# Performance work log

Hardware: AMD Instinct MI355X
Metric: run time of the kernel (lower is better)

The kernel has to match this reference:

```python
import jax, jax.numpy as jnp
import numpy as np

VEC_DIM = 128
N_DOCS = 100000
N_WORDS = 100000
BATCH = 16384
CTX = 8
N_SAMPLES = 6


def setup_inputs() -> dict:
    key = jax.random.key(0)
    k1, k2, k3, k4, k5 = jax.random.split(key, 5)
    doc_ids = jax.random.randint(k1, (BATCH,), 0, N_DOCS, dtype=jnp.int64 if jax.config.jax_enable_x64 else jnp.int32)
    context_ids = jax.random.randint(k2, (BATCH, CTX), 0, N_WORDS)
    sample_ids = jax.random.randint(k3, (BATCH, N_SAMPLES), 0, N_WORDS)
    paragraph_matrix = jax.random.normal(k4, (N_DOCS, VEC_DIM), dtype=jnp.float32)
    word_matrix = jax.random.normal(k5, (N_WORDS, VEC_DIM), dtype=jnp.float32)
    outputs = jnp.zeros((VEC_DIM, N_WORDS), dtype=jnp.float32)
    return {
        "doc_ids": doc_ids,
        "context_ids": context_ids,
        "sample_ids": sample_ids,
        "paragraph_matrix": paragraph_matrix,
        "word_matrix": word_matrix,
        "outputs": outputs,
    }


def reference(doc_ids, context_ids, sample_ids, paragraph_matrix, word_matrix, outputs):
    # concat=False branch of DistributedMemory.forward
    # [B, CTX, D] gathered then summed over context -> [B, D]
    word_sum = jnp.sum(word_matrix[context_ids, :], axis=1)
    doc_vec = paragraph_matrix[doc_ids, :]            # [B, D]
    inputs = doc_vec + word_sum                       # [B, D]
    # outputs[:, sample_ids] -> [D, B, S]; bmm([B,1,D],[B,D,S]) == einsum
    out_cols = outputs[:, sample_ids]                 # [D, B, S]
    logits = jnp.einsum("bd,dbs->bs", inputs, out_cols)  # [B, S]
    return logits
```

## Files before the change

kernel.cpp:

```cpp
#include <hip/hip_runtime.h>
#include <stdint.h>

#define VEC_DIM   128
#define N_WORDS   100000
#define CTX       8
#define N_SAMPLES 6
#define BATCH     16384
#define N_GROUPS  6250
#define TOTAL_S   (BATCH * N_SAMPLES)
#define CAP       64

static constexpr size_t OFF_INPUTS  = 0;
static constexpr size_t OFF_COUNT   = 8388608;
static constexpr size_t OFF_RECORDS = OFF_COUNT + 25024;

__global__ void k_zero(uint32_t* __restrict__ count) {
    int i = blockIdx.x * 256 + threadIdx.x;
    if (i < N_GROUPS) count[i] = 0u;
}

__global__ __launch_bounds__(256) void k_gather_append(
    const int* __restrict__ doc_ids, const int* __restrict__ context_ids,
    const int* __restrict__ sample_ids,
    const float* __restrict__ para, const float* __restrict__ words,
    float* __restrict__ inputs, uint32_t* __restrict__ count,
    uint32_t* __restrict__ records)
{
    const int t    = threadIdx.x;
    const int wave = t >> 6;
    const int lane = t & 63;
    const int b    = blockIdx.x * 4 + wave;

    if (t < 24) {
        int i  = blockIdx.x * 24 + t;
        int id = sample_ids[i];
        int g  = id >> 4;
        uint32_t pos = atomicAdd(&count[g], 1u);
        int bb = i / N_SAMPLES;
        int ss = i - bb * N_SAMPLES;
        if (pos < CAP)
            records[g * CAP + pos] =
                ((uint32_t)bb << 7) | ((uint32_t)ss << 4) | (uint32_t)(id & 15);
    }

    const int doc = doc_ids[b];
    int cids[CTX];
    #pragma unroll
    for (int c = 0; c < CTX; ++c) cids[c] = context_ids[b * CTX + c];

    const float2* prow = reinterpret_cast<const float2*>(para + (size_t)doc * VEC_DIM);
    float2 acc = prow[lane];
    #pragma unroll
    for (int c = 0; c < CTX; ++c) {
        const float2* wrow = reinterpret_cast<const float2*>(words + (size_t)cids[c] * VEC_DIM);
        float2 w = wrow[lane];
        acc.x += w.x; acc.y += w.y;
    }
    reinterpret_cast<float2*>(inputs)[(size_t)b * 64 + lane] = acc;
}

__global__ __launch_bounds__(256) void k_process(
    const float* __restrict__ outs,
    const float* __restrict__ inputs,
    const uint32_t* __restrict__ count,
    const uint32_t* __restrict__ records,
    float* __restrict__ logits)
{
    const int g = blockIdx.x;
    uint32_t n = count[g];
    if (n > CAP) n = CAP;
    if (n == 0) return;

    __shared__ float tileT[16][132];

    const int t = threadIdx.x;
    const int base_col = g * 16;
    #pragma unroll
    for (int k = 0; k < 2; ++k) {
        int idx = t + k * 256;
        int d   = idx >> 2;
        int c4  = idx & 3;
        float4 v = *reinterpret_cast<const float4*>(
            outs + (size_t)d * N_WORDS + base_col + c4 * 4);
        tileT[c4 * 4 + 0][d] = v.x;
        tileT[c4 * 4 + 1][d] = v.y;
        tileT[c4 * 4 + 2][d] = v.z;
        tileT[c4 * 4 + 3][d] = v.w;
    }
    __syncthreads();

    const int slot = t >> 4;
    const int j    = t & 15;

    for (uint32_t i = slot; i < n; i += 16) {
        uint32_t rec = records[g * CAP + i];
        int c = rec & 15;
        int s = (rec >> 4) & 7;
        int b = (int)(rec >> 7);

        const float4* inp4 = reinterpret_cast<const float4*>(inputs + (size_t)b * VEC_DIM);
        float4 a0 = inp4[j * 2];
        float4 a1 = inp4[j * 2 + 1];
        float4 w0 = *reinterpret_cast<const float4*>(&tileT[c][j * 8]);
        float4 w1 = *reinterpret_cast<const float4*>(&tileT[c][j * 8 + 4]);

        float p = a0.x * w0.x + a0.y * w0.y + a0.z * w0.z + a0.w * w0.w
                + a1.x * w1.x + a1.y * w1.y + a1.z * w1.z + a1.w * w1.w;

        #pragma unroll
        for (int off = 1; off < 16; off <<= 1)
            p += __shfl_xor(p, off, 64);

        if (j == 0)
            logits[(size_t)b * N_SAMPLES + s] = p;
    }
}

extern "C" void kernel_launch(void* const* d_in, const int* in_sizes, int n_in,
                              void* d_out, int out_size, void* d_ws, size_t ws_size,
                              hipStream_t stream) {
    const int*   doc_ids     = (const int*)  d_in[0];
    const int*   context_ids = (const int*)  d_in[1];
    const int*   sample_ids  = (const int*)  d_in[2];
    const float* para        = (const float*)d_in[3];
    const float* words       = (const float*)d_in[4];
    const float* outs        = (const float*)d_in[5];
    float*       logits      = (float*)      d_out;

    char* ws = (char*)d_ws;
    float*    inputs  = (float*)   (ws + OFF_INPUTS);
    uint32_t* count   = (uint32_t*)(ws + OFF_COUNT);
    uint32_t* records = (uint32_t*)(ws + OFF_RECORDS);

    hipLaunchKernelGGL(k_zero, dim3((N_GROUPS + 255) / 256), dim3(256), 0, stream, count);
    hipLaunchKernelGGL(k_gather_append, dim3(BATCH / 4), dim3(256), 0, stream,
                       doc_ids, context_ids, sample_ids, para, words,
                       inputs, count, records);
    hipLaunchKernelGGL(k_process, dim3(N_GROUPS), dim3(256), 0, stream,
                       outs, inputs, count, records, logits);
}
```

Baseline: 174.0 us.

## Fuse three kernels into one persistent cooperative kernel with grid syncs and tile prefetch

```diff
diff --git a/kernel.cpp b/kernel.cpp
--- a/kernel.cpp
+++ b/kernel.cpp
@@ -1,5 +1,8 @@
 #include <hip/hip_runtime.h>
+#include <hip/hip_cooperative_groups.h>
 #include <stdint.h>
+
+namespace cg = cooperative_groups;
 
 #define VEC_DIM   128
 #define N_WORDS   100000
@@ -9,10 +12,128 @@
 #define N_GROUPS  6250
 #define TOTAL_S   (BATCH * N_SAMPLES)
 #define CAP       64
+#define GRID      1536
 
 static constexpr size_t OFF_INPUTS  = 0;
 static constexpr size_t OFF_COUNT   = 8388608;
 static constexpr size_t OFF_RECORDS = OFF_COUNT + 25024;
+
+#define TILE_WRITE(buf, idx, v) do {                                   \
+    int d_ = (idx) >> 2, c4_ = (idx) & 3;                              \
+    tileT[buf][c4_ * 4 + 0][d_] = (v).x;                               \
+    tileT[buf][c4_ * 4 + 1][d_] = (v).y;                               \
+    tileT[buf][c4_ * 4 + 2][d_] = (v).z;                               \
+    tileT[buf][c4_ * 4 + 3][d_] = (v).w;                               \
+} while (0)
+
+__global__ __launch_bounds__(256, 6) void k_all(
+    const int* __restrict__ doc_ids, const int* __restrict__ context_ids,
+    const int* __restrict__ sample_ids,
+    const float* __restrict__ para, const float* __restrict__ words,
+    const float* __restrict__ outs,
+    float* __restrict__ inputs, uint32_t* __restrict__ count,
+    uint32_t* __restrict__ records, float* __restrict__ logits)
+{
+    cg::grid_group gg = cg::this_grid();
+    __shared__ float tileT[2][16][132];
+
+    const int t   = threadIdx.x;
+    const int bid = blockIdx.x;
+    const int gid = bid * 256 + t;
+
+    if (gid < N_GROUPS) count[gid] = 0u;
+    gg.sync();
+
+    if (gid < TOTAL_S) {
+        int id = sample_ids[gid];
+        int g  = id >> 4;
+        uint32_t pos = atomicAdd(&count[g], 1u);
+        int bb = gid / N_SAMPLES;
+        int ss = gid - bb * N_SAMPLES;
+        if (pos < CAP)
+            records[g * CAP + pos] =
+                ((uint32_t)bb << 7) | ((uint32_t)ss << 4) | (uint32_t)(id & 15);
+    }
+
+    float4 pf0, pf1;
+    {
+        int i0 = t,      d0 = i0 >> 2, c0 = i0 & 3;
+        int i1 = t + 256, d1 = i1 >> 2, c1 = i1 & 3;
+        pf0 = *reinterpret_cast<const float4*>(outs + (size_t)d0 * N_WORDS + bid * 16 + c0 * 4);
+        pf1 = *reinterpret_cast<const float4*>(outs + (size_t)d1 * N_WORDS + bid * 16 + c1 * 4);
+    }
+
+    const int wave = t >> 6;
+    const int lane = t & 63;
+    for (int base = bid * 4; base < BATCH; base += GRID * 4) {
+        const int b   = base + wave;
+        const int doc = doc_ids[b];
+        int cids[CTX];
+        #pragma unroll
+        for (int c = 0; c < CTX; ++c) cids[c] = context_ids[b * CTX + c];
+
+        const float2* prow = reinterpret_cast<const float2*>(para + (size_t)doc * VEC_DIM);
+        float2 acc = prow[lane];
+        #pragma unroll
+        for (int c = 0; c < CTX; ++c) {
+            const float2* wrow = reinterpret_cast<const float2*>(words + (size_t)cids[c] * VEC_DIM);
+            float2 w = wrow[lane];
+            acc.x += w.x; acc.y += w.y;
+        }
+        reinterpret_cast<float2*>(inputs)[(size_t)b * 64 + lane] = acc;
+    }
+
+    TILE_WRITE(0, t, pf0);
+    TILE_WRITE(0, t + 256, pf1);
+
+    gg.sync();
+
+    const int slot = t >> 4;
+    const int j    = t & 15;
+    int cur = 0;
+    for (int g = bid; g < N_GROUPS; g += GRID) {
+        const int gn = g + GRID;
+        float4 n0, n1;
+        if (gn < N_GROUPS) {
+            int i0 = t,      d0 = i0 >> 2, c0 = i0 & 3;
+            int i1 = t + 256, d1 = i1 >> 2, c1 = i1 & 3;
+            n0 = *reinterpret_cast<const float4*>(outs + (size_t)d0 * N_WORDS + gn * 16 + c0 * 4);
+            n1 = *reinterpret_cast<const float4*>(outs + (size_t)d1 * N_WORDS + gn * 16 + c1 * 4);
+        }
+
+        uint32_t n = count[g];
+        if (n > CAP) n = CAP;
+        for (uint32_t i = slot; i < n; i += 16) {
+            uint32_t rec = records[g * CAP + i];
+            int c = rec & 15;
+            int s = (rec >> 4) & 7;
+            int b = (int)(rec >> 7);
+
+            const float4* inp4 = reinterpret_cast<const float4*>(inputs + (size_t)b * VEC_DIM);
+            float4 a0 = inp4[j * 2];
+            float4 a1 = inp4[j * 2 + 1];
+            float4 w0 = *reinterpret_cast<const float4*>(&tileT[cur][c][j * 8]);
+            float4 w1 = *reinterpret_cast<const float4*>(&tileT[cur][c][j * 8 + 4]);
+
+            float p = a0.x * w0.x + a0.y * w0.y + a0.z * w0.z + a0.w * w0.w
+                    + a1.x * w1.x + a1.y * w1.y + a1.z * w1.z + a1.w * w1.w;
+
+            #pragma unroll
+            for (int off = 1; off < 16; off <<= 1)
+                p += __shfl_xor(p, off, 64);
+
+            if (j == 0)
+                logits[(size_t)b * N_SAMPLES + s] = p;
+        }
+
+        if (gn < N_GROUPS) {
+            TILE_WRITE(cur ^ 1, t, n0);
+            TILE_WRITE(cur ^ 1, t + 256, n1);
+        }
+        __syncthreads();
+        cur ^= 1;
+    }
+}
 
 __global__ void k_zero(uint32_t* __restrict__ count) {
     int i = blockIdx.x * 256 + threadIdx.x;
@@ -72,16 +193,14 @@
     if (n == 0) return;
 
     __shared__ float tileT[16][132];
-
     const int t = threadIdx.x;
-    const int base_col = g * 16;
     #pragma unroll
     for (int k = 0; k < 2; ++k) {
         int idx = t + k * 256;
         int d   = idx >> 2;
         int c4  = idx & 3;
         float4 v = *reinterpret_cast<const float4*>(
-            outs + (size_t)d * N_WORDS + base_col + c4 * 4);
+            outs + (size_t)d * N_WORDS + g * 16 + c4 * 4);
         tileT[c4 * 4 + 0][d] = v.x;
         tileT[c4 * 4 + 1][d] = v.y;
         tileT[c4 * 4 + 2][d] = v.z;
@@ -91,7 +210,6 @@
 
     const int slot = t >> 4;
     const int j    = t & 15;
-
     for (uint32_t i = slot; i < n; i += 16) {
         uint32_t rec = records[g * CAP + i];
         int c = rec & 15;
@@ -132,10 +250,19 @@
     uint32_t* count   = (uint32_t*)(ws + OFF_COUNT);
     uint32_t* records = (uint32_t*)(ws + OFF_RECORDS);
 
-    hipLaunchKernelGGL(k_zero, dim3((N_GROUPS + 255) / 256), dim3(256), 0, stream, count);
-    hipLaunchKernelGGL(k_gather_append, dim3(BATCH / 4), dim3(256), 0, stream,
-                       doc_ids, context_ids, sample_ids, para, words,
-                       inputs, count, records);
-    hipLaunchKernelGGL(k_process, dim3(N_GROUPS), dim3(256), 0, stream,
-                       outs, inputs, count, records, logits);
-}
+    void* args[] = { (void*)&doc_ids, (void*)&context_ids, (void*)&sample_ids,
+                     (void*)&para, (void*)&words, (void*)&outs,
+                     (void*)&inputs, (void*)&count, (void*)&records, (void*)&logits };
+
+    hipError_t err = hipLaunchCooperativeKernel((const void*)k_all, dim3(GRID), dim3(256),
+                                                args, 0, stream);
+    if (err != hipSuccess) {
+        (void)hipGetLastError();
+        hipLaunchKernelGGL(k_zero, dim3((N_GROUPS + 255) / 256), dim3(256), 0, stream, count);
+        hipLaunchKernelGGL(k_gather_append, dim3(BATCH / 4), dim3(256), 0, stream,
+                           doc_ids, context_ids, sample_ids, para, words,
+                           inputs, count, records);
+        hipLaunchKernelGGL(k_process, dim3(N_GROUPS), dim3(256), 0, stream,
+                           outs, inputs, count, records, logits);
+    }
+}
```

Measured after the change: 418.3 us. +140.4%, slower.
